# Kernel optimization log

Hardware: AMD Instinct MI355X
Metric: run time of the kernel (lower is better)

Reference implementation:

```python
import jax, jax.numpy as jnp
import numpy as np

B, N, D, H = 4, 2048, 1024, 16
DH = D // H  # head dim = 64


def positional_encoding(n, dim):
    # Faithful vectorization of the numpy double loop in PositionalEncoding.
    i = jnp.arange(dim)
    even_i = (i % 2) == 0
    denom_i = 10000.0 ** (2.0 * jnp.where(even_i, i, i - 1).astype(jnp.float32) / dim)
    pos = jnp.arange(n, dtype=jnp.float32)[:, None]  # [n,1]
    base = jnp.where(even_i[None, :], jnp.sin(pos / denom_i), jnp.cos(pos / denom_i))  # [n,dim]
    p = jnp.arange(n)
    even_p = (p % 2) == 0
    denom_p = 10000.0 ** (2.0 * jnp.where(even_p, p, p - 1).astype(jnp.float32) / n)  # [n]
    j = jnp.arange(dim, dtype=jnp.float32)[None, :]  # [1,dim]
    mult = jnp.where(even_p[:, None], jnp.sin(j / denom_p[:, None]), jnp.cos(j / denom_p[:, None]))  # [n,dim]
    return base * mult


def setup_inputs() -> dict:
    key = jax.random.key(0)
    ks = jax.random.split(key, 4)
    s = 1.0 / np.sqrt(D)
    return {
        "data": jax.random.normal(ks[0], (B, N, D), dtype=jnp.float32),
        "Wq": jax.random.normal(ks[1], (D, D), dtype=jnp.float32) * s,
        "bq": jnp.zeros((D,), dtype=jnp.float32),
        "Wk": jax.random.normal(ks[2], (D, D), dtype=jnp.float32) * s,
        "bk": jnp.zeros((D,), dtype=jnp.float32),
        "Wv": jax.random.normal(ks[3], (D, D), dtype=jnp.float32) * s,
        "bv": jnp.zeros((D,), dtype=jnp.float32),
    }


def _split_heads(x):
    # tf.concat(tf.split(x, H, axis=-1), axis=0): head-major [H*B, N, DH]
    b, n, d = x.shape
    return x.reshape(b, n, H, DH).transpose(2, 0, 1, 3).reshape(H * b, n, DH)


def reference(data, Wq, bq, Wk, bk, Wv, bv):
    b, n, d = data.shape
    x = data + positional_encoding(n, d).astype(data.dtype)  # [B,N,D]
    q = _split_heads(x @ Wq + bq)  # [H*B,N,DH]
    k = _split_heads(x @ Wk + bk)
    v = _split_heads(x @ Wv + bv)
    # scale uses last dim of key AFTER split, i.e. head_dim
    scores = jnp.einsum('bqd,bkd->bqk', q, k) / jnp.sqrt(jnp.float32(DH))  # [H*B,N,N]
    w = jax.nn.softmax(scores, axis=-1)
    return jnp.einsum('bqk,bkd->bqd', w, v)  # [H*B,N,DH]
```

## Files before the change

kernel.cpp:

```cpp
#include <hip/hip_runtime.h>
#include <hip/hip_bf16.h>

#define BB 4
#define NN 2048
#define DD 1024
#define HH 16
#define DHH 64
#define HB (HH*BB)

typedef __bf16 bf16;
typedef __bf16 bf16x4v __attribute__((ext_vector_type(4)));
typedef __bf16 bf16x8 __attribute__((ext_vector_type(8)));
typedef float f32x4 __attribute__((ext_vector_type(4)));
typedef float f32x16 __attribute__((ext_vector_type(16)));
typedef unsigned u32x2 __attribute__((ext_vector_type(2)));

#if __has_builtin(__builtin_amdgcn_permlane32_swap)
#define HAVE_PLSWAP 1
#else
#define HAVE_PLSWAP 0
#endif

#define QSCALE 0.18033688011112042f

__device__ __forceinline__ void async16(const void* g, void* l) {
    __builtin_amdgcn_global_load_lds(
        (const __attribute__((address_space(1))) unsigned int*)g,
        (__attribute__((address_space(3))) unsigned int*)l, 16, 0, 0);
}

__device__ __forceinline__ unsigned pkbf(float a, float b) {
    union { bf16 h[2]; unsigned u; } x;
    x.h[0] = (bf16)a; x.h[1] = (bf16)b;
    return x.u;
}

__global__ void pe_add_kernel(const float* __restrict__ data, bf16* __restrict__ xb) {
    int t = blockIdx.x * blockDim.x + threadIdx.x;
    int base = t * 4;
    int row = base >> 10;
    int d0 = base & 1023;
    int n = row & (NN - 1);
    const float LOG2_10000 = 13.287712379549449f;
    int pn = n & ~1;
    float denom_p = __builtin_amdgcn_exp2f((2.0f * (float)pn / (float)NN) * LOG2_10000);
    bool even_p = (n & 1) == 0;
    float4 dv = *(const float4*)(data + base);
    float din[4] = {dv.x, dv.y, dv.z, dv.w};
    bf16x4v ov;
    #pragma unroll
    for (int u = 0; u < 4; ++u) {
        int d = d0 + u;
        int di = d & ~1;
        float denom_i = __builtin_amdgcn_exp2f((2.0f * (float)di / (float)DD) * LOG2_10000);
        float a = (float)n / denom_i;
        float basev = ((d & 1) == 0) ? __sinf(a) : __cosf(a);
        float bm = (float)d / denom_p;
        float mult = even_p ? __sinf(bm) : __cosf(bm);
        ov[u] = (bf16)(din[u] + basev * mult);
    }
    *(bf16x4v*)(xb + base) = ov;
}

__global__ void wtrans_kernel(const float* __restrict__ Wq, const float* __restrict__ Wk,
                              const float* __restrict__ Wv, bf16* __restrict__ Bw) {
    const float* W = (blockIdx.z == 0) ? Wq : (blockIdx.z == 1) ? Wk : Wv;
    bf16* Wt = Bw + (size_t)blockIdx.z * 1024 * 1024;
    __shared__ float s[32][33];
    int bx = blockIdx.x * 32;
    int by = blockIdx.y * 32;
    int tx = threadIdx.x, ty = threadIdx.y;
    #pragma unroll
    for (int i = 0; i < 32; i += 8)
        s[ty + i][tx] = W[(by + ty + i) * DD + bx + tx];
    __syncthreads();
    #pragma unroll
    for (int i = 0; i < 32; i += 8)
        Wt[(size_t)(bx + ty + i) * DD + by + tx] = (bf16)s[tx][ty + i];
}

__launch_bounds__(256)
__global__ void gemm_qkv_fused(const bf16* __restrict__ A,
                               const bf16* __restrict__ Bw,
                               const float* __restrict__ bq, const float* __restrict__ bk,
                               const float* __restrict__ bv,
                               bf16* __restrict__ Qs, bf16* __restrict__ Ks,
                               bf16* __restrict__ Vb) {
    __shared__ char smem[36864];
    int tid = threadIdx.x;
    int w = tid >> 6, lane = tid & 63, l32 = lane & 31, hi = lane >> 5;
    int bi = blockIdx.x;
    int bn = bi >> 6;
    int bm = (bi & 7) * 8 + ((bi >> 3) & 7);
    int m0 = bm * 128, n0 = bn * 128;
    int wm = (w & 1) * 64, wn = (w >> 1) * 64;

    int srow = tid >> 2;
    int g4 = (tid & 3) ^ (srow & 3);
    const bf16* aS0 = A + (size_t)(m0 + srow) * DD + g4 * 8;
    const bf16* aS1 = aS0 + (size_t)64 * DD;
    const bf16* bS0 = Bw + (size_t)(n0 + srow) * DD + g4 * 8;
    const bf16* bS1 = bS0 + (size_t)64 * DD;

    f32x16 acc[2][2];
    #pragma unroll
    for (int i = 0; i < 2; ++i)
        #pragma unroll
        for (int j = 0; j < 2; ++j)
            #pragma unroll
            for (int r = 0; r < 16; ++r) acc[i][j][r] = 0.f;

    async16(aS0, smem + w * 1024);
    async16(aS1, smem + 4096 + w * 1024);
    async16(bS0, smem + 8192 + w * 1024);
    async16(bS1, smem + 12288 + w * 1024);
    __syncthreads();

    for (int kk = 0; kk < DD; kk += 32) {
        char* buf  = smem + ((kk >> 5) & 1) * 16384;
        char* nbuf = smem + (((kk >> 5) & 1) ^ 1) * 16384;
        if (kk + 32 < DD) {
            async16(aS0 + kk + 32, nbuf + w * 1024);
            async16(aS1 + kk + 32, nbuf + 4096 + w * 1024);
            async16(bS0 + kk + 32, nbuf + 8192 + w * 1024);
            async16(bS1 + kk + 32, nbuf + 12288 + w * 1024);
        }
        const char* As = buf;
        const char* Bs = buf + 8192;
        bf16x8 af[2][2], bfr[2][2];
        #pragma unroll
        for (int mt = 0; mt < 2; ++mt) {
            int row = wm + mt * 32 + l32;
            #pragma unroll
            for (int kc = 0; kc < 2; ++kc)
                af[mt][kc] = *(const bf16x8*)(As + row * 64 + ((kc * 2 + hi) ^ (l32 & 3)) * 16);
        }
        #pragma unroll
        for (int nt = 0; nt < 2; ++nt) {
            int row = wn + nt * 32 + l32;
            #pragma unroll
            for (int kc = 0; kc < 2; ++kc)
                bfr[nt][kc] = *(const bf16x8*)(Bs + row * 64 + ((kc * 2 + hi) ^ (l32 & 3)) * 16);
        }
        #pragma unroll
        for (int mt = 0; mt < 2; ++mt)
            #pragma unroll
            for (int nt = 0; nt < 2; ++nt)
                #pragma unroll
                for (int kc = 0; kc < 2; ++kc)
                    acc[mt][nt] = __builtin_amdgcn_mfma_f32_32x32x16_bf16(
                        af[mt][kc], bfr[nt][kc], acc[mt][nt], 0, 0, 0);
        __syncthreads();
    }

    int mat = n0 >> 10;
    if (mat < 2) {
        const float* bias_p = (mat == 0) ? bq : bk;
        #pragma unroll
        for (int nt = 0; nt < 2; ++nt) {
            int ncol = (n0 + wn + nt * 32 + l32) & 1023;
            float bias = bias_p[ncol];
            int h = ncol >> 6, dh = ncol & 63;
            #pragma unroll
            for (int mt = 0; mt < 2; ++mt) {
                int rowbase = m0 + wm + mt * 32 + 4 * hi;
                #pragma unroll
                for (int m4 = 0; m4 < 4; ++m4) {
                    #pragma unroll
                    for (int rr = 0; rr < 4; ++rr) {
                        int mrow = rowbase + 8 * m4 + rr;
                        int b_ = mrow >> 11, nn_ = mrow & 2047;
                        int hbi = h * BB + b_;
                        float v = acc[mt][nt][m4 * 4 + rr] + bias;
                        if (mat == 0)
                            Qs[((size_t)hbi * NN + nn_) * DHH + dh] = (bf16)(v * QSCALE);
                        else
                            Ks[((size_t)hbi * NN + nn_) * DHH + dh] = (bf16)v;
                    }
                }
            }
        }
    } else {
        bf16* vl = (bf16*)smem;
        #pragma unroll
        for (int nt = 0; nt < 2; ++nt) {
            int ncol_l = wn + nt * 32 + l32;
            float bias = bv[(n0 + ncol_l) & 1023];
            #pragma unroll
            for (int mt = 0; mt < 2; ++mt) {
                int m_base = wm + mt * 32 + 4 * hi;
                #pragma unroll
                for (int m4 = 0; m4 < 4; ++m4) {
                    bf16x4v q;
                    #pragma unroll
                    for (int rr = 0; rr < 4; ++rr)
                        q[rr] = (bf16)(acc[mt][nt][m4 * 4 + rr] + bias);
                    *(bf16x4v*)(vl + ncol_l * 130 + m_base + 8 * m4) = q;
                }
            }
        }
        __syncthreads();
        int b_ = m0 >> 11, nn0 = m0 & 2047;
        #pragma unroll
        for (int p = 0; p < 2; ++p) {
            int ncol = p * 64 + (tid >> 2);
            int ncg = (n0 + ncol) & 1023;
            int h = ncg >> 6, dh = ncg & 63;
            bf16* dst = Vb + ((size_t)(h * BB + b_) * DHH + dh) * NN + nn0;
            #pragma unroll
            for (int i = 0; i < 4; ++i) {
                int eoff = ((tid & 3) + 4 * i) * 8;
                bf16x8 vv = *(const bf16x8*)(vl + ncol * 130 + eoff);
                *(bf16x8*)(dst + eoff) = vv;
            }
        }
    }
}

__launch_bounds__(256, 3)
__global__ void attn_kernel(const bf16* __restrict__ Qs,
                            const bf16* __restrict__ Ks,
                            const bf16* __restrict__ Vb,
                            float* __restrict__ out) {
    __shared__ char smem[33280];
    int tid = threadIdx.x;
    int w = tid >> 6, lane = tid & 63, l32 = lane & 31, hi = lane >> 5;
    int qh = w & 1, kh = w >> 1;
    int bi = blockIdx.x;
    int xcd = bi & 7, jj = bi >> 3;
    int hb = xcd * 8 + (jj & 7);
    int qb = jj >> 3;
    int q0 = qb * 128;

    bf16x8 qf[2][4];
    #pragma unroll
    for (int qs = 0; qs < 2; ++qs) {
        const bf16* qbase = Qs + ((size_t)hb * NN + q0 + qh * 64 + qs * 32 + l32) * DHH + hi * 8;
        #pragma unroll
        for (int c = 0; c < 4; ++c)
            qf[qs][c] = *(const bf16x8*)(qbase + c * 16);
    }

    int srow = tid >> 3;
    int g8 = (tid & 7) ^ (srow & 7);
    const bf16* ksrc = Ks + ((size_t)hb * NN + srow) * DHH + g8 * 8;
    const bf16* vsrc = Vb + ((size_t)hb * DHH + srow) * NN + g8 * 8;

    f32x16 o[2][2];
    #pragma unroll
    for (int qs = 0; qs < 2; ++qs)
        #pragma unroll
        for (int d = 0; d < 2; ++d)
            #pragma unroll
            for (int r = 0; r < 16; ++r) o[qs][d][r] = 0.f;
    float ts[2] = {0.f, 0.f};

    async16(ksrc,            smem + w * 1024);
    async16(ksrc + 32 * 64,  smem + 4096 + w * 1024);
    async16(vsrc,            smem + 8192 + w * 1024);
    async16(vsrc + 32 * NN,  smem + 12288 + w * 1024);
    __syncthreads();

    for (int kt = 0; kt < NN; kt += 64) {
        char* buf  = smem + ((kt >> 6) & 1) * 16384;
        char* nbuf = smem + (((kt >> 6) & 1) ^ 1) * 16384;
        if (kt + 64 < NN) {
            async16(ksrc + (size_t)(kt + 64) * 64,      nbuf + w * 1024);
            async16(ksrc + (size_t)(kt + 96) * 64,      nbuf + 4096 + w * 1024);
            async16(vsrc + (kt + 64),                   nbuf + 8192 + w * 1024);
            async16(vsrc + (size_t)32 * NN + (kt + 64), nbuf + 12288 + w * 1024);
        }
        const char* ktile = buf;
        const char* vtile = buf + 8192;

        bf16x8 kf[4];
        int krow = kh * 32 + l32;
        #pragma unroll
        for (int c = 0; c < 4; ++c)
            kf[c] = *(const bf16x8*)(ktile + krow * 128 + ((c * 2 + hi) ^ (l32 & 7)) * 16);

        f32x16 sa[2];
        #pragma unroll
        for (int qs = 0; qs < 2; ++qs) {
            #pragma unroll
            for (int r = 0; r < 16; ++r) sa[qs][r] = 0.f;
            #pragma unroll
            for (int c = 0; c < 4; ++c)
                sa[qs] = __builtin_amdgcn_mfma_f32_32x32x16_bf16(kf[c], qf[qs][c], sa[qs], 0, 0, 0);
        }

        unsigned dw[2][4][2];
        #pragma unroll
        for (int qs = 0; qs < 2; ++qs) {
            float t0 = 0.f;
            #pragma unroll
            for (int m4 = 0; m4 < 4; ++m4) {
                float p0 = __builtin_amdgcn_exp2f(sa[qs][m4 * 4 + 0]);
                float p1 = __builtin_amdgcn_exp2f(sa[qs][m4 * 4 + 1]);
                float p2 = __builtin_amdgcn_exp2f(sa[qs][m4 * 4 + 2]);
                float p3 = __builtin_amdgcn_exp2f(sa[qs][m4 * 4 + 3]);
                t0 += (p0 + p1) + (p2 + p3);
                dw[qs][m4][0] = pkbf(p0, p1);
                dw[qs][m4][1] = pkbf(p2, p3);
            }
            ts[qs] += t0;
        }

        #pragma unroll
        for (int kc = 0; kc < 2; ++kc) {
            bf16x8 vf[2];
            #pragma unroll
            for (int d = 0; d < 2; ++d) {
                int vrow = d * 32 + l32;
                vf[d] = *(const bf16x8*)(vtile + vrow * 128 +
                                         ((kh * 4 + kc * 2 + hi) ^ (l32 & 7)) * 16);
            }
            #pragma unroll
            for (int qs = 0; qs < 2; ++qs) {
                int mlo = kc * 2;
                unsigned a0 = dw[qs][mlo][0],     a1 = dw[qs][mlo][1];
                unsigned b0 = dw[qs][mlo + 1][0], b1 = dw[qs][mlo + 1][1];
                union { unsigned u[4]; bf16x8 v; } pu;
#if HAVE_PLSWAP
                u32x2 r0 = __builtin_amdgcn_permlane32_swap(a0, b0, false, false);
                u32x2 r1 = __builtin_amdgcn_permlane32_swap(a1, b1, false, false);
                pu.u[0] = r0.x; pu.u[1] = r1.x; pu.u[2] = r0.y; pu.u[3] = r1.y;
#else
                unsigned own0 = hi ? b0 : a0, own1 = hi ? b1 : a1;
                unsigned snd0 = hi ? a0 : b0, snd1 = hi ? a1 : b1;
                unsigned rcv0 = __shfl_xor(snd0, 32, 64);
                unsigned rcv1 = __shfl_xor(snd1, 32, 64);
                pu.u[0] = hi ? rcv0 : own0;
                pu.u[1] = hi ? rcv1 : own1;
                pu.u[2] = hi ? own0 : rcv0;
                pu.u[3] = hi ? own1 : rcv1;
#endif
                #pragma unroll
                for (int d = 0; d < 2; ++d)
                    o[qs][d] = __builtin_amdgcn_mfma_f32_32x32x16_bf16(vf[d], pu.v, o[qs][d], 0, 0, 0);
            }
        }
        __syncthreads();
    }

    float* Osm = (float*)smem;
    float* Ls  = (float*)(smem + 32768);
    float tsq[2];
    #pragma unroll
    for (int qs = 0; qs < 2; ++qs)
        tsq[qs] = ts[qs] + __shfl_xor(ts[qs], 32, 64);

    if (kh == 0) {
        #pragma unroll
        for (int qs = 0; qs < 2; ++qs) {
            int q_l = qh * 64 + qs * 32 + l32;
            #pragma unroll
            for (int d = 0; d < 2; ++d)
                #pragma unroll
                for (int m4 = 0; m4 < 4; ++m4) {
                    int ci = d * 8 + m4 * 2 + hi;
                    int pc = ci ^ (q_l & 15);
                    f32x4 v;
                    v[0] = o[qs][d][m4 * 4 + 0];
                    v[1] = o[qs][d][m4 * 4 + 1];
                    v[2] = o[qs][d][m4 * 4 + 2];
                    v[3] = o[qs][d][m4 * 4 + 3];
                    *(f32x4*)(Osm + q_l * 64 + pc * 4) = v;
                }
            if (!hi) Ls[q_l] = tsq[qs];
        }
    }
    __syncthreads();
    if (kh == 1) {
        #pragma unroll
        for (int qs = 0; qs < 2; ++qs) {
            int q_l = qh * 64 + qs * 32 + l32;
            #pragma unroll
            for (int d = 0; d < 2; ++d)
                #pragma unroll
                for (int m4 = 0; m4 < 4; ++m4) {
                    int ci = d * 8 + m4 * 2 + hi;
                    int pc = ci ^ (q_l & 15);
                    f32x4 v = *(const f32x4*)(Osm + q_l * 64 + pc * 4);
                    v[0] += o[qs][d][m4 * 4 + 0];
                    v[1] += o[qs][d][m4 * 4 + 1];
                    v[2] += o[qs][d][m4 * 4 + 2];
                    v[3] += o[qs][d][m4 * 4 + 3];
                    *(f32x4*)(Osm + q_l * 64 + pc * 4) = v;
                }
            if (!hi) Ls[q_l] += tsq[qs];
        }
    }
    __syncthreads();
    float* outb = out + ((size_t)hb * NN + q0) * DHH;
    #pragma unroll
    for (int i = 0; i < 8; ++i) {
        int g = tid + 256 * i;
        int q_l = g >> 4, ci = g & 15;
        int pc = ci ^ (q_l & 15);
        float inv = 1.0f / Ls[q_l];
        f32x4 v = *(const f32x4*)(Osm + q_l * 64 + pc * 4);
        v *= inv;
        *(f32x4*)(outb + g * 4) = v;
    }
}

extern "C" void kernel_launch(void* const* d_in, const int* in_sizes, int n_in,
                              void* d_out, int out_size, void* d_ws, size_t ws_size,
                              hipStream_t stream) {
    const float* data = (const float*)d_in[0];
    const float* Wq   = (const float*)d_in[1];
    const float* bq   = (const float*)d_in[2];
    const float* Wk   = (const float*)d_in[3];
    const float* bk   = (const float*)d_in[4];
    const float* Wv   = (const float*)d_in[5];
    const float* bv   = (const float*)d_in[6];
    float* out = (float*)d_out;

    char* ws = (char*)d_ws;
    bf16* xb = (bf16*)ws; ws += (size_t)8192 * 1024 * 2;
    bf16* Bw = (bf16*)ws; ws += (size_t)3072 * 1024 * 2;
    bf16* Qs = (bf16*)ws; ws += (size_t)HB * NN * DHH * 2;
    bf16* Ks = (bf16*)ws; ws += (size_t)HB * NN * DHH * 2;
    bf16* Vb = (bf16*)ws; ws += (size_t)HB * NN * DHH * 2;

    pe_add_kernel<<<8192, 256, 0, stream>>>(data, xb);
    dim3 tb(32, 8), tg(32, 32, 3);
    wtrans_kernel<<<tg, tb, 0, stream>>>(Wq, Wk, Wv, Bw);
    gemm_qkv_fused<<<1536, 256, 0, stream>>>(xb, Bw, bq, bk, bv, Qs, Ks, Vb);
    attn_kernel<<<1024, 256, 0, stream>>>(Qs, Ks, Vb, out);
}
```

Baseline: 260.1 us.

## Rewrite QKV GEMM with 256x256 tiles, 8 waves, phased async pipeline

Replaces the 128x128, 4-wave QKV projection GEMM with a 256x256 tile, 8-wave (512-thread) kernel that uses 128KB of dynamic shared memory, 64-wide K steps split into four phases, and double buffering with explicit vmcnt waits and priority boosts around the MFMA bursts. The larger tile raises operand reuse and lowers global/L2 traffic per FLOP, and the phased barriers let loads overlap with compute. The trade-off is only 384 blocks at one block per CU, which can leave CUs idle and expose more of the tail, and the epilogue now does the V transpose in two rounds.

```diff
diff --git a/kernel.cpp b/kernel.cpp
--- a/kernel.cpp
+++ b/kernel.cpp
@@ -79,140 +79,169 @@
         Wt[(size_t)(bx + ty + i) * DD + by + tx] = (bf16)s[tx][ty + i];
 }
 
-__launch_bounds__(256)
-__global__ void gemm_qkv_fused(const bf16* __restrict__ A,
-                               const bf16* __restrict__ Bw,
-                               const float* __restrict__ bq, const float* __restrict__ bk,
-                               const float* __restrict__ bv,
-                               bf16* __restrict__ Qs, bf16* __restrict__ Ks,
-                               bf16* __restrict__ Vb) {
-    __shared__ char smem[36864];
+__launch_bounds__(512)
+__global__ void gemm_qkv_8ph(const bf16* __restrict__ A,
+                             const bf16* __restrict__ Bw,
+                             const float* __restrict__ bq, const float* __restrict__ bk,
+                             const float* __restrict__ bv,
+                             bf16* __restrict__ Qs, bf16* __restrict__ Ks,
+                             bf16* __restrict__ Vb) {
+    extern __shared__ char smem[];
     int tid = threadIdx.x;
     int w = tid >> 6, lane = tid & 63, l32 = lane & 31, hi = lane >> 5;
     int bi = blockIdx.x;
-    int bn = bi >> 6;
-    int bm = (bi & 7) * 8 + ((bi >> 3) & 7);
-    int m0 = bm * 128, n0 = bn * 128;
-    int wm = (w & 1) * 64, wn = (w >> 1) * 64;
-
-    int srow = tid >> 2;
-    int g4 = (tid & 3) ^ (srow & 3);
-    const bf16* aS0 = A + (size_t)(m0 + srow) * DD + g4 * 8;
-    const bf16* aS1 = aS0 + (size_t)64 * DD;
-    const bf16* bS0 = Bw + (size_t)(n0 + srow) * DD + g4 * 8;
-    const bf16* bS1 = bS0 + (size_t)64 * DD;
-
-    f32x16 acc[2][2];
-    #pragma unroll
-    for (int i = 0; i < 2; ++i)
-        #pragma unroll
-        for (int j = 0; j < 2; ++j)
-            #pragma unroll
-            for (int r = 0; r < 16; ++r) acc[i][j][r] = 0.f;
-
-    async16(aS0, smem + w * 1024);
-    async16(aS1, smem + 4096 + w * 1024);
-    async16(bS0, smem + 8192 + w * 1024);
-    async16(bS1, smem + 12288 + w * 1024);
-    __syncthreads();
-
-    for (int kk = 0; kk < DD; kk += 32) {
-        char* buf  = smem + ((kk >> 5) & 1) * 16384;
-        char* nbuf = smem + (((kk >> 5) & 1) ^ 1) * 16384;
-        if (kk + 32 < DD) {
-            async16(aS0 + kk + 32, nbuf + w * 1024);
-            async16(aS1 + kk + 32, nbuf + 4096 + w * 1024);
-            async16(bS0 + kk + 32, nbuf + 8192 + w * 1024);
-            async16(bS1 + kk + 32, nbuf + 12288 + w * 1024);
-        }
-        const char* As = buf;
-        const char* Bs = buf + 8192;
-        bf16x8 af[2][2], bfr[2][2];
-        #pragma unroll
-        for (int mt = 0; mt < 2; ++mt) {
-            int row = wm + mt * 32 + l32;
-            #pragma unroll
-            for (int kc = 0; kc < 2; ++kc)
-                af[mt][kc] = *(const bf16x8*)(As + row * 64 + ((kc * 2 + hi) ^ (l32 & 3)) * 16);
-        }
-        #pragma unroll
-        for (int nt = 0; nt < 2; ++nt) {
-            int row = wn + nt * 32 + l32;
-            #pragma unroll
-            for (int kc = 0; kc < 2; ++kc)
-                bfr[nt][kc] = *(const bf16x8*)(Bs + row * 64 + ((kc * 2 + hi) ^ (l32 & 3)) * 16);
-        }
-        #pragma unroll
-        for (int mt = 0; mt < 2; ++mt)
-            #pragma unroll
-            for (int nt = 0; nt < 2; ++nt)
-                #pragma unroll
-                for (int kc = 0; kc < 2; ++kc)
-                    acc[mt][nt] = __builtin_amdgcn_mfma_f32_32x32x16_bf16(
-                        af[mt][kc], bfr[nt][kc], acc[mt][nt], 0, 0, 0);
-        __syncthreads();
-    }
-
-    int mat = n0 >> 10;
+    int swz = (bi & 7) * 48 + (bi >> 3);
+    int bm = swz & 31, bn = swz >> 5;
+    int m0 = bm * 256, n0 = bn * 256;
+    int wm = (w >> 2) * 128, wn = (w & 3) * 64;
+
+    int tid16 = tid * 16;
+    int cb8 = ((tid & 1) ^ ((tid >> 3) & 1)) * 8;
+    const bf16* sA0 = A  + (size_t)(m0 + (tid >> 1)) * DD + cb8;
+    const bf16* sB0 = Bw + (size_t)(n0 + (tid >> 1)) * DD + cb8;
+
+    int flip = (hi ^ ((l32 >> 2) & 1)) << 4;
+    int abase = (wm + l32) * 32 + flip;
+    int bbase = (wn + l32) * 32 + flip;
+
+    f32x16 acc[4][2];
+    #pragma unroll
+    for (int fr = 0; fr < 4; ++fr)
+        #pragma unroll
+        for (int cn = 0; cn < 2; ++cn)
+            #pragma unroll
+            for (int r = 0; r < 16; ++r) acc[fr][cn][r] = 0.f;
+
+    #pragma unroll
+    for (int p = 0; p < 4; ++p) {
+        async16(sA0 + p * 16, smem + p * 8192 + tid16);
+        async16(sB0 + p * 16, smem + 32768 + p * 8192 + tid16);
+    }
+    asm volatile("s_waitcnt vmcnt(6)" ::: "memory");
+    __builtin_amdgcn_s_barrier();
+
+    const int NT = DD / 64;
+    for (int t = 0; t < NT - 1; ++t) {
+        const char* sb = smem + (t & 1) * 65536;
+        char* nxt = smem + ((t & 1) ^ 1) * 65536;
+        int kt1 = (t + 1) << 6;
+        #pragma unroll
+        for (int p = 0; p < 4; ++p) {
+            bf16x8 afr[4], bfv[2];
+            #pragma unroll
+            for (int fr = 0; fr < 4; ++fr)
+                afr[fr] = *(const bf16x8*)(sb + p * 8192 + abase + fr * 1024);
+            #pragma unroll
+            for (int cn = 0; cn < 2; ++cn)
+                bfv[cn] = *(const bf16x8*)(sb + 32768 + p * 8192 + bbase + cn * 1024);
+            async16(sA0 + kt1 + p * 16, nxt + p * 8192 + tid16);
+            async16(sB0 + kt1 + p * 16, nxt + 32768 + p * 8192 + tid16);
+            __builtin_amdgcn_s_barrier();
+            __builtin_amdgcn_s_setprio(1);
+            #pragma unroll
+            for (int fr = 0; fr < 4; ++fr)
+                #pragma unroll
+                for (int cn = 0; cn < 2; ++cn)
+                    acc[fr][cn] = __builtin_amdgcn_mfma_f32_32x32x16_bf16(
+                        afr[fr], bfv[cn], acc[fr][cn], 0, 0, 0);
+            __builtin_amdgcn_s_setprio(0);
+            asm volatile("s_waitcnt vmcnt(6)" ::: "memory");
+            __builtin_amdgcn_s_barrier();
+        }
+    }
+    {
+        const char* sb = smem + ((NT - 1) & 1) * 65536;
+        #pragma unroll
+        for (int p = 0; p < 4; ++p) {
+            bf16x8 afr[4], bfv[2];
+            #pragma unroll
+            for (int fr = 0; fr < 4; ++fr)
+                afr[fr] = *(const bf16x8*)(sb + p * 8192 + abase + fr * 1024);
+            #pragma unroll
+            for (int cn = 0; cn < 2; ++cn)
+                bfv[cn] = *(const bf16x8*)(sb + 32768 + p * 8192 + bbase + cn * 1024);
+            __builtin_amdgcn_s_barrier();
+            __builtin_amdgcn_s_setprio(1);
+            #pragma unroll
+            for (int fr = 0; fr < 4; ++fr)
+                #pragma unroll
+                for (int cn = 0; cn < 2; ++cn)
+                    acc[fr][cn] = __builtin_amdgcn_mfma_f32_32x32x16_bf16(
+                        afr[fr], bfv[cn], acc[fr][cn], 0, 0, 0);
+            __builtin_amdgcn_s_setprio(0);
+            if (p == 0) asm volatile("s_waitcnt vmcnt(4)" ::: "memory");
+            if (p == 1) asm volatile("s_waitcnt vmcnt(2)" ::: "memory");
+            if (p == 2) asm volatile("s_waitcnt vmcnt(0)" ::: "memory");
+            __builtin_amdgcn_s_barrier();
+        }
+    }
+
+    int mat = bn >> 2;
+    int nb = (bn & 3) * 256;
     if (mat < 2) {
         const float* bias_p = (mat == 0) ? bq : bk;
         #pragma unroll
-        for (int nt = 0; nt < 2; ++nt) {
-            int ncol = (n0 + wn + nt * 32 + l32) & 1023;
-            float bias = bias_p[ncol];
-            int h = ncol >> 6, dh = ncol & 63;
-            #pragma unroll
-            for (int mt = 0; mt < 2; ++mt) {
-                int rowbase = m0 + wm + mt * 32 + 4 * hi;
+        for (int cn = 0; cn < 2; ++cn) {
+            int nc = nb + wn + cn * 32 + l32;
+            float bias = bias_p[nc];
+            int h = nc >> 6, dh = nc & 63;
+            #pragma unroll
+            for (int fr = 0; fr < 4; ++fr) {
+                int rowbase = m0 + wm + fr * 32 + 4 * hi;
                 #pragma unroll
                 for (int m4 = 0; m4 < 4; ++m4) {
                     #pragma unroll
                     for (int rr = 0; rr < 4; ++rr) {
-                        int mrow = rowbase + 8 * m4 + rr;
-                        int b_ = mrow >> 11, nn_ = mrow & 2047;
-                        int hbi = h * BB + b_;
-                        float v = acc[mt][nt][m4 * 4 + rr] + bias;
+                        int m = rowbase + 8 * m4 + rr;
+                        int b_ = m >> 11, nn_ = m & 2047;
+                        float v = acc[fr][cn][m4 * 4 + rr] + bias;
                         if (mat == 0)
-                            Qs[((size_t)hbi * NN + nn_) * DHH + dh] = (bf16)(v * QSCALE);
+                            Qs[((size_t)(h * BB + b_) * NN + nn_) * DHH + dh] = (bf16)(v * QSCALE);
                         else
-                            Ks[((size_t)hbi * NN + nn_) * DHH + dh] = (bf16)v;
+                            Ks[((size_t)(h * BB + b_) * NN + nn_) * DHH + dh] = (bf16)v;
                     }
                 }
             }
         }
     } else {
         bf16* vl = (bf16*)smem;
-        #pragma unroll
-        for (int nt = 0; nt < 2; ++nt) {
-            int ncol_l = wn + nt * 32 + l32;
-            float bias = bv[(n0 + ncol_l) & 1023];
-            #pragma unroll
-            for (int mt = 0; mt < 2; ++mt) {
-                int m_base = wm + mt * 32 + 4 * hi;
-                #pragma unroll
-                for (int m4 = 0; m4 < 4; ++m4) {
-                    bf16x4v q;
+        int b_ = m0 >> 11, nn0 = m0 & 2047;
+        #pragma unroll
+        for (int r = 0; r < 2; ++r) {
+            __syncthreads();
+            if ((w >> 2) == r) {
+                #pragma unroll
+                for (int cn = 0; cn < 2; ++cn) {
+                    int col = wn + cn * 32 + l32;
+                    float bias = bv[nb + col];
                     #pragma unroll
-                    for (int rr = 0; rr < 4; ++rr)
-                        q[rr] = (bf16)(acc[mt][nt][m4 * 4 + rr] + bias);
-                    *(bf16x4v*)(vl + ncol_l * 130 + m_base + 8 * m4) = q;
+                    for (int fr = 0; fr < 4; ++fr) {
+                        int mb = fr * 32 + 4 * hi;
+                        #pragma unroll
+                        for (int m4 = 0; m4 < 4; ++m4) {
+                            bf16x4v q;
+                            #pragma unroll
+                            for (int rr = 0; rr < 4; ++rr)
+                                q[rr] = (bf16)(acc[fr][cn][m4 * 4 + rr] + bias);
+                            *(bf16x4v*)(vl + col * 130 + mb + 8 * m4) = q;
+                        }
+                    }
                 }
             }
-        }
-        __syncthreads();
-        int b_ = m0 >> 11, nn0 = m0 & 2047;
-        #pragma unroll
-        for (int p = 0; p < 2; ++p) {
-            int ncol = p * 64 + (tid >> 2);
-            int ncg = (n0 + ncol) & 1023;
-            int h = ncg >> 6, dh = ncg & 63;
-            bf16* dst = Vb + ((size_t)(h * BB + b_) * DHH + dh) * NN + nn0;
-            #pragma unroll
-            for (int i = 0; i < 4; ++i) {
-                int eoff = ((tid & 3) + 4 * i) * 8;
-                bf16x8 vv = *(const bf16x8*)(vl + ncol * 130 + eoff);
-                *(bf16x8*)(dst + eoff) = vv;
-            }
+            __syncthreads();
+            #pragma unroll
+            for (int pass = 0; pass < 2; ++pass) {
+                int col = pass * 128 + (tid >> 2);
+                int nc = nb + col;
+                int h = nc >> 6, dh = nc & 63;
+                bf16* dst = Vb + ((size_t)(h * BB + b_) * DHH + dh) * NN + nn0 + r * 128;
+                #pragma unroll
+                for (int i = 0; i < 4; ++i) {
+                    int eoff = ((tid & 3) + 4 * i) * 8;
+                    *(bf16x8*)(dst + eoff) = *(const bf16x8*)(vl + col * 130 + eoff);
+                }
+            }
+            __syncthreads();
         }
     }
 }
@@ -424,9 +453,16 @@
     bf16* Ks = (bf16*)ws; ws += (size_t)HB * NN * DHH * 2;
     bf16* Vb = (bf16*)ws; ws += (size_t)HB * NN * DHH * 2;
 
+    static bool attr_done = false;
+    if (!attr_done) {
+        hipFuncSetAttribute((const void*)gemm_qkv_8ph,
+                            hipFuncAttributeMaxDynamicSharedMemorySize, 131072);
+        attr_done = true;
+    }
+
     pe_add_kernel<<<8192, 256, 0, stream>>>(data, xb);
     dim3 tb(32, 8), tg(32, 32, 3);
     wtrans_kernel<<<tg, tb, 0, stream>>>(Wq, Wk, Wv, Bw);
-    gemm_qkv_fused<<<1536, 256, 0, stream>>>(xb, Bw, bq, bk, bv, Qs, Ks, Vb);
+    gemm_qkv_8ph<<<384, 512, 131072, stream>>>(xb, Bw, bq, bk, bv, Qs, Ks, Vb);
     attn_kernel<<<1024, 256, 0, stream>>>(Qs, Ks, Vb, out);
 }
```

After: 280.6 us. +7.9%, slower.

## Use triple-buffered K/V tiles with two-deep async prefetch in attention

Applied to the files above, without the earlier changes.

Moves the attention kernel's K/V staging from double to triple buffering in LDS, with prefetch running two tiles ahead. The full __syncthreads at the end of each iteration becomes a partial s_waitcnt vmcnt(4) plus a barrier, so the most recent prefetch can stay in flight while the next tile is computed. This hides more global-load latency. LDS per block grows from about 33KB to about 49.6KB, which can lower occupancy (launch bounds ask for 3 blocks/CU), and correctness depends on the hand-counted vmcnt values.

```diff
diff --git a/kernel.cpp b/kernel.cpp
--- a/kernel.cpp
+++ b/kernel.cpp
@@ -222,7 +222,7 @@
                             const bf16* __restrict__ Ks,
                             const bf16* __restrict__ Vb,
                             float* __restrict__ out) {
-    __shared__ char smem[33280];
+    __shared__ char smem[49664];
     int tid = threadIdx.x;
     int w = tid >> 6, lane = tid & 63, l32 = lane & 31, hi = lane >> 5;
     int qh = w & 1, kh = w >> 1;
@@ -255,20 +255,32 @@
             for (int r = 0; r < 16; ++r) o[qs][d][r] = 0.f;
     float ts[2] = {0.f, 0.f};
 
-    async16(ksrc,            smem + w * 1024);
-    async16(ksrc + 32 * 64,  smem + 4096 + w * 1024);
-    async16(vsrc,            smem + 8192 + w * 1024);
-    async16(vsrc + 32 * NN,  smem + 12288 + w * 1024);
-    __syncthreads();
-
+    {
+        char* b0 = smem;
+        char* b1 = smem + 16384;
+        async16(ksrc,                      b0 + w * 1024);
+        async16(ksrc + 32 * 64,            b0 + 4096 + w * 1024);
+        async16(vsrc,                      b0 + 8192 + w * 1024);
+        async16(vsrc + (size_t)32 * NN,    b0 + 12288 + w * 1024);
+        async16(ksrc + 64 * 64,            b1 + w * 1024);
+        async16(ksrc + 96 * 64,            b1 + 4096 + w * 1024);
+        async16(vsrc + 64,                 b1 + 8192 + w * 1024);
+        async16(vsrc + (size_t)32 * NN + 64, b1 + 12288 + w * 1024);
+    }
+    asm volatile("s_waitcnt vmcnt(4)" ::: "memory");
+    __builtin_amdgcn_s_barrier();
+
+    int bsel = 0;
     for (int kt = 0; kt < NN; kt += 64) {
-        char* buf  = smem + ((kt >> 6) & 1) * 16384;
-        char* nbuf = smem + (((kt >> 6) & 1) ^ 1) * 16384;
-        if (kt + 64 < NN) {
-            async16(ksrc + (size_t)(kt + 64) * 64,      nbuf + w * 1024);
-            async16(ksrc + (size_t)(kt + 96) * 64,      nbuf + 4096 + w * 1024);
-            async16(vsrc + (kt + 64),                   nbuf + 8192 + w * 1024);
-            async16(vsrc + (size_t)32 * NN + (kt + 64), nbuf + 12288 + w * 1024);
+        char* buf = smem + bsel * 16384;
+        bool pf = (kt + 128) < NN;
+        if (pf) {
+            int pb = bsel + 2; if (pb >= 3) pb -= 3;
+            char* nbuf = smem + pb * 16384;
+            async16(ksrc + (size_t)(kt + 128) * 64,      nbuf + w * 1024);
+            async16(ksrc + (size_t)(kt + 160) * 64,      nbuf + 4096 + w * 1024);
+            async16(vsrc + (kt + 128),                   nbuf + 8192 + w * 1024);
+            async16(vsrc + (size_t)32 * NN + (kt + 128), nbuf + 12288 + w * 1024);
         }
         const char* ktile = buf;
         const char* vtile = buf + 8192;
@@ -340,11 +352,16 @@
                     o[qs][d] = __builtin_amdgcn_mfma_f32_32x32x16_bf16(vf[d], pu.v, o[qs][d], 0, 0, 0);
             }
         }
-        __syncthreads();
-    }
+
+        if (pf) asm volatile("s_waitcnt vmcnt(4)" ::: "memory");
+        else    asm volatile("s_waitcnt vmcnt(0)" ::: "memory");
+        __builtin_amdgcn_s_barrier();
+        bsel = bsel + 1; if (bsel >= 3) bsel = 0;
+    }
+    __syncthreads();
 
     float* Osm = (float*)smem;
-    float* Ls  = (float*)(smem + 32768);
+    float* Ls  = (float*)(smem + 49152);
     float tsq[2];
     #pragma unroll
     for (int qs = 0; qs < 2; ++qs)
```

New measurement: 248.2 us. 1.05x faster.

## Load K/V fragments directly from global memory, dropping LDS staging and barriers

Applied to the files above, without the earlier changes.

The attention loop stops staging K and V tiles through double-buffered shared memory with async copies and per-iteration barriers. Each wave now loads its MFMA operand fragments straight from global memory, prefetching the next K fragment into registers after the QK MFMAs. This removes LDS traffic and the __syncthreads on every key tile. In exchange, data that waves previously shared through LDS is fetched redundantly from global/L2, and V loads are issued without prefetch, which can expose memory latency.

```diff
diff --git a/kernel.cpp b/kernel.cpp
--- a/kernel.cpp
+++ b/kernel.cpp
@@ -241,10 +241,8 @@
             qf[qs][c] = *(const bf16x8*)(qbase + c * 16);
     }
 
-    int srow = tid >> 3;
-    int g8 = (tid & 7) ^ (srow & 7);
-    const bf16* ksrc = Ks + ((size_t)hb * NN + srow) * DHH + g8 * 8;
-    const bf16* vsrc = Vb + ((size_t)hb * DHH + srow) * NN + g8 * 8;
+    const bf16* kbase = Ks + ((size_t)hb * NN + kh * 32 + l32) * DHH + hi * 8;
+    const bf16* vbase = Vb + ((size_t)hb * DHH + l32) * NN + kh * 32 + hi * 8;
 
     f32x16 o[2][2];
     #pragma unroll
@@ -255,29 +253,18 @@
             for (int r = 0; r < 16; ++r) o[qs][d][r] = 0.f;
     float ts[2] = {0.f, 0.f};
 
-    async16(ksrc,            smem + w * 1024);
-    async16(ksrc + 32 * 64,  smem + 4096 + w * 1024);
-    async16(vsrc,            smem + 8192 + w * 1024);
-    async16(vsrc + 32 * NN,  smem + 12288 + w * 1024);
-    __syncthreads();
+    bf16x8 kf[4];
+    #pragma unroll
+    for (int c = 0; c < 4; ++c)
+        kf[c] = *(const bf16x8*)(kbase + c * 16);
 
     for (int kt = 0; kt < NN; kt += 64) {
-        char* buf  = smem + ((kt >> 6) & 1) * 16384;
-        char* nbuf = smem + (((kt >> 6) & 1) ^ 1) * 16384;
-        if (kt + 64 < NN) {
-            async16(ksrc + (size_t)(kt + 64) * 64,      nbuf + w * 1024);
-            async16(ksrc + (size_t)(kt + 96) * 64,      nbuf + 4096 + w * 1024);
-            async16(vsrc + (kt + 64),                   nbuf + 8192 + w * 1024);
-            async16(vsrc + (size_t)32 * NN + (kt + 64), nbuf + 12288 + w * 1024);
-        }
-        const char* ktile = buf;
-        const char* vtile = buf + 8192;
-
-        bf16x8 kf[4];
-        int krow = kh * 32 + l32;
-        #pragma unroll
-        for (int c = 0; c < 4; ++c)
-            kf[c] = *(const bf16x8*)(ktile + krow * 128 + ((c * 2 + hi) ^ (l32 & 7)) * 16);
+        bf16x8 vf[2][2];
+        #pragma unroll
+        for (int kc = 0; kc < 2; ++kc)
+            #pragma unroll
+            for (int d = 0; d < 2; ++d)
+                vf[kc][d] = *(const bf16x8*)(vbase + (size_t)d * 32 * NN + kt + kc * 16);
 
         f32x16 sa[2];
         #pragma unroll
@@ -287,6 +274,12 @@
             #pragma unroll
             for (int c = 0; c < 4; ++c)
                 sa[qs] = __builtin_amdgcn_mfma_f32_32x32x16_bf16(kf[c], qf[qs][c], sa[qs], 0, 0, 0);
+        }
+
+        if (kt + 64 < NN) {
+            #pragma unroll
+            for (int c = 0; c < 4; ++c)
+                kf[c] = *(const bf16x8*)(kbase + (size_t)(kt + 64) * DHH + c * 16);
         }
 
         unsigned dw[2][4][2];
@@ -308,13 +301,6 @@
 
         #pragma unroll
         for (int kc = 0; kc < 2; ++kc) {
-            bf16x8 vf[2];
-            #pragma unroll
-            for (int d = 0; d < 2; ++d) {
-                int vrow = d * 32 + l32;
-                vf[d] = *(const bf16x8*)(vtile + vrow * 128 +
-                                         ((kh * 4 + kc * 2 + hi) ^ (l32 & 7)) * 16);
-            }
             #pragma unroll
             for (int qs = 0; qs < 2; ++qs) {
                 int mlo = kc * 2;
@@ -337,10 +323,9 @@
 #endif
                 #pragma unroll
                 for (int d = 0; d < 2; ++d)
-                    o[qs][d] = __builtin_amdgcn_mfma_f32_32x32x16_bf16(vf[d], pu.v, o[qs][d], 0, 0, 0);
+                    o[qs][d] = __builtin_amdgcn_mfma_f32_32x32x16_bf16(vf[kc][d], pu.v, o[qs][d], 0, 0, 0);
             }
         }
-        __syncthreads();
     }
 
     float* Osm = (float*)smem;
```

Result: slower. 437.3 us (+68.1%).
